# Kernel optimization log

Hardware: AMD Instinct MI355X
Metric: run time of the kernel (lower is better)

The kernel has to match this reference:

```python
import jax, jax.numpy as jnp
import numpy as np

LN_EPS = 1e-5

def _layernorm(x, scale, bias):
    mu = jnp.mean(x, axis=-1, keepdims=True)
    var = jnp.var(x, axis=-1, keepdims=True)
    return (x - mu) * jax.lax.rsqrt(var + LN_EPS) * scale + bias

def setup_inputs() -> dict:
    T, node_num, num_nodes, E, C = 4, 10000, 50000, 256, 128
    key = jax.random.key(0)
    ks = jax.random.split(key, 12)
    s = lambda fan_in: 1.0 / np.sqrt(fan_in)
    return {
        "x": jax.random.normal(ks[0], (T * node_num, E), jnp.float32),
        "batched_x": jax.random.normal(ks[1], (num_nodes, E), jnp.float32),
        "indices": jax.random.randint(ks[2], (T, node_num), 0, num_nodes, jnp.int32),
        "ln_d_scale": jnp.ones((E,), jnp.float32),
        "ln_d_bias": jnp.zeros((E,), jnp.float32),
        "W1_d": jax.random.normal(ks[3], (E, 2 * E), jnp.float32) * s(E),
        "b1_d": jnp.zeros((2 * E,), jnp.float32),
        "W2_d": jax.random.normal(ks[4], (2 * E, C), jnp.float32) * s(2 * E),
        "b2_d": jnp.zeros((C,), jnp.float32),
        "ln_u_scale": jnp.ones((C,), jnp.float32),
        "ln_u_bias": jnp.zeros((C,), jnp.float32),
        "W1_u": jax.random.normal(ks[5], (C, 2 * C), jnp.float32) * s(C),
        "b1_u": jnp.zeros((2 * C,), jnp.float32),
        "W2_u": jax.random.normal(ks[6], (2 * C, E), jnp.float32) * s(2 * C),
        "b2_u": jnp.zeros((E,), jnp.float32),
    }

def reference(x, batched_x, indices, ln_d_scale, ln_d_bias, W1_d, b1_d, W2_d, b2_d,
              ln_u_scale, ln_u_bias, W1_u, b1_u, W2_u, b2_u):
    T, node_num = indices.shape
    num_nodes, E = batched_x.shape
    xr = x.reshape(T, node_num, E)
    # _to_entire: per-step scatter-add of active-node embeddings into the full node table
    def scatter_one(xi, idx):
        return jnp.zeros((num_nodes, E), x.dtype).at[idx].add(xi)
    ta = jax.vmap(scatter_one)(xr, indices)          # [T, num_nodes, E]
    inp = ta + batched_x[None]                        # broadcast entire features
    h = _layernorm(inp, ln_d_scale, ln_d_bias)
    h = jax.nn.gelu(h @ W1_d + b1_d, approximate=False) @ W2_d + b2_d  # [T, num_nodes, C]
    # _from_entire: gather each step's active nodes back, concat, LN + MLP up
    g = jnp.take_along_axis(h, indices[..., None], axis=1)  # [T, node_num, C]
    g = g.reshape(T * node_num, -1)
    g = _layernorm(g, ln_u_scale, ln_u_bias)
    out = jax.nn.gelu(g @ W1_u + b1_u, approximate=False) @ W2_u + b2_u  # [T*node_num, E]
    return out
```

## Files before the change

### kernel.cpp

```cpp
#include <hip/hip_runtime.h>
#include <math.h>

#define T_STEPS   4
#define NODE_NUM  10000
#define NUM_NODES 50000
#define E         256
#define TWO_E     512
#define CC        128
#define TWO_C     256
#define ROWS      32

typedef short bf16x8 __attribute__((ext_vector_type(8)));
typedef float f32x4  __attribute__((ext_vector_type(4)));

#define MFMA16(a, b, c) __builtin_amdgcn_mfma_f32_16x16x32_bf16((a), (b), (c), 0, 0, 0)

static __device__ unsigned short g_wt[294912];

__device__ __forceinline__ float geluf(float v) {
    return 0.5f * v * (1.0f + erff(v * 0.70710678118654752440f));
}

__device__ __forceinline__ unsigned short f2bf(float f) {
    unsigned int u = __builtin_bit_cast(unsigned int, f);
    u += 0x7fffu + ((u >> 16) & 1u);
    return (unsigned short)(u >> 16);
}

__global__ void prep_weights(const float* __restrict__ W1d, const float* __restrict__ W2d,
                             const float* __restrict__ W1u, const float* __restrict__ W2u) {
    int i = blockIdx.x * 256 + threadIdx.x;
    if (i < 131072) {
        int n = i >> 8, k = i & 255;
        g_wt[i] = f2bf(W1d[(size_t)k * TWO_E + n]);
    }
    if (i < 65536) {
        int n = i >> 9, k = i & 511;
        g_wt[131072 + i] = f2bf(W2d[(size_t)k * CC + n]);
    }
    if (i < 32768) {
        int n = i >> 7, k = i & 127;
        g_wt[196608 + i] = f2bf(W1u[(size_t)k * TWO_C + n]);
    }
    if (i < 65536) {
        int n = i >> 8, k = i & 255;
        g_wt[229376 + i] = f2bf(W2u[(size_t)k * E + n]);
    }
}

__global__ void zero_rows_kernel(float* __restrict__ table,
                                 const int* __restrict__ indices,
                                 int gr0, int t0) {
    int gr = gr0 + blockIdx.x * 4 + (threadIdx.x >> 6);
    int trel = gr / NODE_NUM - t0;
    int idx = indices[gr];
    int c = (threadIdx.x & 63) * 4;
    float4 z = make_float4(0.f, 0.f, 0.f, 0.f);
    *reinterpret_cast<float4*>(&table[((size_t)trel * NUM_NODES + idx) * E + c]) = z;
}

__global__ void scatter_kernel(float* __restrict__ table,
                               const float* __restrict__ x,
                               const int* __restrict__ indices,
                               int gr0, int t0) {
    int gr = gr0 + blockIdx.x;
    int trel = gr / NODE_NUM - t0;
    int idx = indices[gr];
    atomicAdd(&table[((size_t)trel * NUM_NODES + idx) * E + threadIdx.x],
              x[(size_t)gr * E + threadIdx.x]);
}

__global__ __launch_bounds__(256, 3)
void mlp_kernel(const float* __restrict__ table,
                const float* __restrict__ batched_x,
                const int* __restrict__ indices,
                const float* __restrict__ lnd_s, const float* __restrict__ lnd_b,
                const float* __restrict__ b1d, const float* __restrict__ b2d,
                const float* __restrict__ lnu_s, const float* __restrict__ lnu_b,
                const float* __restrict__ b1u, const float* __restrict__ b2u,
                float* __restrict__ out,
                int gr0, int t0, int grLim) {
    __shared__ __align__(16) unsigned char smem[50176];
    __shared__ size_t rbase[ROWS];
    __shared__ int    ridx[ROWS];

    float*          Xf  = (float*)smem;
    unsigned short* Xs  = (unsigned short*)(smem + 33280);
    unsigned short* H1  = (unsigned short*)smem;
    float*          H2f = (float*)(smem + 33280);
    unsigned short* H2b = (unsigned short*)smem;
    unsigned short* G1  = (unsigned short*)(smem + 8704);

    const unsigned short* w1t  = g_wt;
    const unsigned short* w2t  = g_wt + 131072;
    const unsigned short* w1ut = g_wt + 196608;
    const unsigned short* w2ut = g_wt + 229376;

    const int tid = threadIdx.x;
    const int w = tid >> 6, lane = tid & 63;
    const int l16 = lane & 15, quad = lane >> 4;
    const int grb = gr0 + blockIdx.x * ROWS;

    if (tid < ROWS) {
        int gr = grb + tid;
        if (gr >= grLim) gr = grLim - 1;
        int trel = gr / NODE_NUM - t0;
        int idx = indices[gr];
        rbase[tid] = ((size_t)trel * NUM_NODES + idx) * E;
        ridx[tid]  = idx;
    }
    __syncthreads();

    #pragma unroll
    for (int it = 0; it < 8; ++it) {
        int v = it * 256 + tid;
        int r = v >> 6;
        int c = (v & 63) * 4;
        float4 tv = *reinterpret_cast<const float4*>(&table[rbase[r] + c]);
        float4 bv = *reinterpret_cast<const float4*>(&batched_x[(size_t)ridx[r] * E + c]);
        float4 s; s.x = tv.x + bv.x; s.y = tv.y + bv.y; s.z = tv.z + bv.z; s.w = tv.w + bv.w;
        *reinterpret_cast<float4*>(&Xf[r * 260 + c]) = s;
    }
    __syncthreads();

    {
        int row = tid >> 3, l8 = tid & 7;
        float s = 0.f, sq = 0.f;
        #pragma unroll
        for (int k = 0; k < 32; ++k) {
            float v = Xf[row * 260 + k * 8 + l8];
            s += v; sq += v * v;
        }
        s  += __shfl_xor(s, 1);  s  += __shfl_xor(s, 2);  s  += __shfl_xor(s, 4);
        sq += __shfl_xor(sq, 1); sq += __shfl_xor(sq, 2); sq += __shfl_xor(sq, 4);
        float mu = s * (1.0f / E);
        float var = sq * (1.0f / E) - mu * mu;
        float rs = rsqrtf(var + 1e-5f);
        #pragma unroll
        for (int k = 0; k < 32; ++k) {
            int c = k * 8 + l8;
            float v = (Xf[row * 260 + c] - mu) * rs * lnd_s[c] + lnd_b[c];
            Xs[row * 264 + c] = f2bf(v);
        }
    }
    __syncthreads();

    {
        bf16x8 af[2][8];
        #pragma unroll
        for (int mt = 0; mt < 2; ++mt) {
            const unsigned short* base = Xs + (l16 + 16 * mt) * 264 + quad * 8;
            #pragma unroll
            for (int ks = 0; ks < 8; ++ks)
                af[mt][ks] = *reinterpret_cast<const bf16x8*>(base + ks * 32);
        }
        #pragma unroll
        for (int nt_ = 0; nt_ < 8; ++nt_) {
            int n = (w * 8 + nt_) * 16 + l16;
            const unsigned short* bp = w1t + (size_t)n * 256 + quad * 8;
            f32x4 a0 = {0.f, 0.f, 0.f, 0.f}, a1 = {0.f, 0.f, 0.f, 0.f};
            #pragma unroll
            for (int ks = 0; ks < 8; ++ks) {
                bf16x8 b = *reinterpret_cast<const bf16x8*>(bp + ks * 32);
                a0 = MFMA16(af[0][ks], b, a0);
                a1 = MFMA16(af[1][ks], b, a1);
            }
            float bias = b1d[n];
            #pragma unroll
            for (int reg = 0; reg < 4; ++reg) {
                int r = quad * 4 + reg;
                H1[r * 520 + n]        = f2bf(geluf(a0[reg] + bias));
                H1[(r + 16) * 520 + n] = f2bf(geluf(a1[reg] + bias));
            }
        }
    }
    __syncthreads();

    {
        f32x4 acc2[2][2];
        #pragma unroll
        for (int i = 0; i < 2; ++i)
            #pragma unroll
            for (int j = 0; j < 2; ++j) acc2[i][j] = (f32x4){0.f, 0.f, 0.f, 0.f};
        #pragma unroll
        for (int kh = 0; kh < 2; ++kh) {
            bf16x8 af2[2][8];
            #pragma unroll
            for (int mt = 0; mt < 2; ++mt) {
                const unsigned short* base = H1 + (l16 + 16 * mt) * 520 + kh * 256 + quad * 8;
                #pragma unroll
                for (int ks = 0; ks < 8; ++ks)
                    af2[mt][ks] = *reinterpret_cast<const bf16x8*>(base + ks * 32);
            }
            #pragma unroll
            for (int nt2 = 0; nt2 < 2; ++nt2) {
                int n = (w * 2 + nt2) * 16 + l16;
                const unsigned short* bp = w2t + (size_t)n * 512 + kh * 256 + quad * 8;
                #pragma unroll
                for (int ks = 0; ks < 8; ++ks) {
                    bf16x8 b = *reinterpret_cast<const bf16x8*>(bp + ks * 32);
                    acc2[nt2][0] = MFMA16(af2[0][ks], b, acc2[nt2][0]);
                    acc2[nt2][1] = MFMA16(af2[1][ks], b, acc2[nt2][1]);
                }
            }
        }
        #pragma unroll
        for (int nt2 = 0; nt2 < 2; ++nt2) {
            int n = (w * 2 + nt2) * 16 + l16;
            float bias = b2d[n];
            #pragma unroll
            for (int mt = 0; mt < 2; ++mt)
                #pragma unroll
                for (int reg = 0; reg < 4; ++reg) {
                    int r = mt * 16 + quad * 4 + reg;
                    H2f[r * 132 + n] = acc2[nt2][mt][reg] + bias;
                }
        }
    }
    __syncthreads();

    {
        int row = tid >> 3, l8 = tid & 7;
        float s = 0.f, sq = 0.f;
        #pragma unroll
        for (int k = 0; k < 16; ++k) {
            float v = H2f[row * 132 + k * 8 + l8];
            s += v; sq += v * v;
        }
        s  += __shfl_xor(s, 1);  s  += __shfl_xor(s, 2);  s  += __shfl_xor(s, 4);
        sq += __shfl_xor(sq, 1); sq += __shfl_xor(sq, 2); sq += __shfl_xor(sq, 4);
        float mu = s * (1.0f / CC);
        float var = sq * (1.0f / CC) - mu * mu;
        float rs = rsqrtf(var + 1e-5f);
        #pragma unroll
        for (int k = 0; k < 16; ++k) {
            int c = k * 8 + l8;
            float v = (H2f[row * 132 + c] - mu) * rs * lnu_s[c] + lnu_b[c];
            H2b[row * 136 + c] = f2bf(v);
        }
    }
    __syncthreads();

    {
        bf16x8 af3[2][4];
        #pragma unroll
        for (int mt = 0; mt < 2; ++mt) {
            const unsigned short* base = H2b + (l16 + 16 * mt) * 136 + quad * 8;
            #pragma unroll
            for (int ks = 0; ks < 4; ++ks)
                af3[mt][ks] = *reinterpret_cast<const bf16x8*>(base + ks * 32);
        }
        #pragma unroll
        for (int nt_ = 0; nt_ < 4; ++nt_) {
            int n = (w * 4 + nt_) * 16 + l16;
            const unsigned short* bp = w1ut + (size_t)n * 128 + quad * 8;
            f32x4 a0 = {0.f, 0.f, 0.f, 0.f}, a1 = {0.f, 0.f, 0.f, 0.f};
            #pragma unroll
            for (int ks = 0; ks < 4; ++ks) {
                bf16x8 b = *reinterpret_cast<const bf16x8*>(bp + ks * 32);
                a0 = MFMA16(af3[0][ks], b, a0);
                a1 = MFMA16(af3[1][ks], b, a1);
            }
            float bias = b1u[n];
            #pragma unroll
            for (int reg = 0; reg < 4; ++reg) {
                int r = quad * 4 + reg;
                G1[r * 264 + n]        = f2bf(geluf(a0[reg] + bias));
                G1[(r + 16) * 264 + n] = f2bf(geluf(a1[reg] + bias));
            }
        }
    }
    __syncthreads();

    {
        bf16x8 af4[2][8];
        #pragma unroll
        for (int mt = 0; mt < 2; ++mt) {
            const unsigned short* base = G1 + (l16 + 16 * mt) * 264 + quad * 8;
            #pragma unroll
            for (int ks = 0; ks < 8; ++ks)
                af4[mt][ks] = *reinterpret_cast<const bf16x8*>(base + ks * 32);
        }
        #pragma unroll
        for (int nt_ = 0; nt_ < 4; ++nt_) {
            int n = (w * 4 + nt_) * 16 + l16;
            const unsigned short* bp = w2ut + (size_t)n * 256 + quad * 8;
            f32x4 a0 = {0.f, 0.f, 0.f, 0.f}, a1 = {0.f, 0.f, 0.f, 0.f};
            #pragma unroll
            for (int ks = 0; ks < 8; ++ks) {
                bf16x8 b = *reinterpret_cast<const bf16x8*>(bp + ks * 32);
                a0 = MFMA16(af4[0][ks], b, a0);
                a1 = MFMA16(af4[1][ks], b, a1);
            }
            float bias = b2u[n];
            #pragma unroll
            for (int reg = 0; reg < 4; ++reg) {
                int r = quad * 4 + reg;
                int g0 = grb + r, g1 = grb + r + 16;
                if (g0 < grLim) out[(size_t)g0 * E + n] = a0[reg] + bias;
                if (g1 < grLim) out[(size_t)g1 * E + n] = a1[reg] + bias;
            }
        }
    }
}

extern "C" void kernel_launch(void* const* d_in, const int* in_sizes, int n_in,
                              void* d_out, int out_size, void* d_ws, size_t ws_size,
                              hipStream_t stream) {
    const float* x     = (const float*)d_in[0];
    const float* bx    = (const float*)d_in[1];
    const int*   idxp  = (const int*)  d_in[2];
    const float* lnd_s = (const float*)d_in[3];
    const float* lnd_b = (const float*)d_in[4];
    const float* W1d   = (const float*)d_in[5];
    const float* b1d   = (const float*)d_in[6];
    const float* W2d   = (const float*)d_in[7];
    const float* b2d   = (const float*)d_in[8];
    const float* lnu_s = (const float*)d_in[9];
    const float* lnu_b = (const float*)d_in[10];
    const float* W1u   = (const float*)d_in[11];
    const float* b1u   = (const float*)d_in[12];
    const float* W2u   = (const float*)d_in[13];
    const float* b2u   = (const float*)d_in[14];
    float* out = (float*)d_out;
    float* table = (float*)d_ws;

    const size_t slice_bytes = (size_t)NUM_NODES * E * sizeof(float);
    int tb = (int)(ws_size / slice_bytes);
    if (tb < 1) tb = 1;
    if (tb > T_STEPS) tb = T_STEPS;

    prep_weights<<<512, 256, 0, stream>>>(W1d, W2d, W1u, W2u);

    for (int t0 = 0; t0 < T_STEPS; t0 += tb) {
        int tcur = T_STEPS - t0 < tb ? T_STEPS - t0 : tb;
        int nrows = tcur * NODE_NUM;
        int gr0 = t0 * NODE_NUM;
        int grLim = gr0 + nrows;
        zero_rows_kernel<<<nrows / 4, 256, 0, stream>>>(table, idxp, gr0, t0);
        scatter_kernel  <<<nrows, E, 0, stream>>>(table, x, idxp, gr0, t0);
        mlp_kernel<<<(nrows + ROWS - 1) / ROWS, 256, 0, stream>>>(
            table, bx, idxp, lnd_s, lnd_b, b1d, b2d,
            lnu_s, lnu_b, b1u, b2u, out, gr0, t0, grLim);
    }
}
```

Measured before the change: 301.7 us.

## Count index multiplicity to skip scatter table for unique nodes

Adds a per-step histogram of node indices. Rows whose node appears only once read their embedding straight from x in the MLP kernel, and only duplicated nodes are zeroed and atomically accumulated into the workspace table. With random indices most nodes are unique, so this is meant to remove most of the zeroing, atomic traffic and table reads. In exchange it adds a counting kernel, a global count array and an extra count lookup per row.

```diff
diff --git a/kernel.cpp b/kernel.cpp
--- a/kernel.cpp
+++ b/kernel.cpp
@@ -16,6 +16,7 @@
 #define MFMA16(a, b, c) __builtin_amdgcn_mfma_f32_16x16x32_bf16((a), (b), (c), 0, 0, 0)
 
 static __device__ unsigned short g_wt[294912];
+static __device__ int g_cnt[T_STEPS * NUM_NODES];
 
 __device__ __forceinline__ float geluf(float v) {
     return 0.5f * v * (1.0f + erff(v * 0.70710678118654752440f));
@@ -30,6 +31,7 @@
 __global__ void prep_weights(const float* __restrict__ W1d, const float* __restrict__ W2d,
                              const float* __restrict__ W1u, const float* __restrict__ W2u) {
     int i = blockIdx.x * 256 + threadIdx.x;
+    if (i < T_STEPS * NUM_NODES) g_cnt[i] = 0;
     if (i < 131072) {
         int n = i >> 8, k = i & 255;
         g_wt[i] = f2bf(W1d[(size_t)k * TWO_E + n]);
@@ -48,30 +50,41 @@
     }
 }
 
-__global__ void zero_rows_kernel(float* __restrict__ table,
-                                 const int* __restrict__ indices,
-                                 int gr0, int t0) {
+__global__ void count_kernel(const int* __restrict__ indices) {
+    int gr = blockIdx.x * 256 + threadIdx.x;
+    if (gr < T_STEPS * NODE_NUM) {
+        int t = gr / NODE_NUM;
+        atomicAdd(&g_cnt[t * NUM_NODES + indices[gr]], 1);
+    }
+}
+
+__global__ void zero_dup_kernel(float* __restrict__ table,
+                                const int* __restrict__ indices,
+                                int gr0, int t0) {
     int gr = gr0 + blockIdx.x * 4 + (threadIdx.x >> 6);
-    int trel = gr / NODE_NUM - t0;
+    int t = gr / NODE_NUM;
     int idx = indices[gr];
+    if (g_cnt[t * NUM_NODES + idx] < 2) return;
     int c = (threadIdx.x & 63) * 4;
     float4 z = make_float4(0.f, 0.f, 0.f, 0.f);
-    *reinterpret_cast<float4*>(&table[((size_t)trel * NUM_NODES + idx) * E + c]) = z;
-}
-
-__global__ void scatter_kernel(float* __restrict__ table,
-                               const float* __restrict__ x,
-                               const int* __restrict__ indices,
-                               int gr0, int t0) {
+    *reinterpret_cast<float4*>(&table[((size_t)(t - t0) * NUM_NODES + idx) * E + c]) = z;
+}
+
+__global__ void scatter_dup_kernel(float* __restrict__ table,
+                                   const float* __restrict__ x,
+                                   const int* __restrict__ indices,
+                                   int gr0, int t0) {
     int gr = gr0 + blockIdx.x;
-    int trel = gr / NODE_NUM - t0;
+    int t = gr / NODE_NUM;
     int idx = indices[gr];
-    atomicAdd(&table[((size_t)trel * NUM_NODES + idx) * E + threadIdx.x],
+    if (g_cnt[t * NUM_NODES + idx] < 2) return;
+    atomicAdd(&table[((size_t)(t - t0) * NUM_NODES + idx) * E + threadIdx.x],
               x[(size_t)gr * E + threadIdx.x]);
 }
 
 __global__ __launch_bounds__(256, 3)
 void mlp_kernel(const float* __restrict__ table,
+                const float* __restrict__ x,
                 const float* __restrict__ batched_x,
                 const int* __restrict__ indices,
                 const float* __restrict__ lnd_s, const float* __restrict__ lnd_b,
@@ -81,7 +94,7 @@
                 float* __restrict__ out,
                 int gr0, int t0, int grLim) {
     __shared__ __align__(16) unsigned char smem[50176];
-    __shared__ size_t rbase[ROWS];
+    __shared__ const float* rptr[ROWS];
     __shared__ int    ridx[ROWS];
 
     float*          Xf  = (float*)smem;
@@ -104,10 +117,12 @@
     if (tid < ROWS) {
         int gr = grb + tid;
         if (gr >= grLim) gr = grLim - 1;
-        int trel = gr / NODE_NUM - t0;
+        int t = gr / NODE_NUM;
         int idx = indices[gr];
-        rbase[tid] = ((size_t)trel * NUM_NODES + idx) * E;
-        ridx[tid]  = idx;
+        ridx[tid] = idx;
+        rptr[tid] = (g_cnt[t * NUM_NODES + idx] > 1)
+            ? (table + ((size_t)(t - t0) * NUM_NODES + idx) * E)
+            : (x + (size_t)gr * E);
     }
     __syncthreads();
 
@@ -116,7 +131,7 @@
         int v = it * 256 + tid;
         int r = v >> 6;
         int c = (v & 63) * 4;
-        float4 tv = *reinterpret_cast<const float4*>(&table[rbase[r] + c]);
+        float4 tv = *reinterpret_cast<const float4*>(rptr[r] + c);
         float4 bv = *reinterpret_cast<const float4*>(&batched_x[(size_t)ridx[r] * E + c]);
         float4 s; s.x = tv.x + bv.x; s.y = tv.y + bv.y; s.z = tv.z + bv.z; s.w = tv.w + bv.w;
         *reinterpret_cast<float4*>(&Xf[r * 260 + c]) = s;
@@ -330,17 +345,18 @@
     if (tb < 1) tb = 1;
     if (tb > T_STEPS) tb = T_STEPS;
 
-    prep_weights<<<512, 256, 0, stream>>>(W1d, W2d, W1u, W2u);
+    prep_weights<<<784, 256, 0, stream>>>(W1d, W2d, W1u, W2u);
+    count_kernel<<<(T_STEPS * NODE_NUM + 255) / 256, 256, 0, stream>>>(idxp);
 
     for (int t0 = 0; t0 < T_STEPS; t0 += tb) {
         int tcur = T_STEPS - t0 < tb ? T_STEPS - t0 : tb;
         int nrows = tcur * NODE_NUM;
         int gr0 = t0 * NODE_NUM;
         int grLim = gr0 + nrows;
-        zero_rows_kernel<<<nrows / 4, 256, 0, stream>>>(table, idxp, gr0, t0);
-        scatter_kernel  <<<nrows, E, 0, stream>>>(table, x, idxp, gr0, t0);
+        zero_dup_kernel   <<<nrows / 4, 256, 0, stream>>>(table, idxp, gr0, t0);
+        scatter_dup_kernel<<<nrows, E, 0, stream>>>(table, x, idxp, gr0, t0);
         mlp_kernel<<<(nrows + ROWS - 1) / ROWS, 256, 0, stream>>>(
-            table, bx, idxp, lnd_s, lnd_b, b1d, b2d,
+            table, x, bx, idxp, lnd_s, lnd_b, b1d, b2d,
             lnu_s, lnu_b, b1u, b2u, out, gr0, t0, grLim);
     }
 }
```

After: 293.0 us. -2.9%, faster.
